# Kernel optimization log

Hardware: AMD Instinct MI355X
Metric: run time of the kernel (lower is better)

## Reference

```python
import jax, jax.numpy as jnp
import numpy as np

B, S, H0G, H1G, H0E, H1E, A, E = 16384, 512, 512, 256, 1024, 512, 64, 4


def setup_inputs() -> dict:
    key = jax.random.key(0)
    ks = jax.random.split(key, 8)
    rn = lambda k, shape, s=0.05: jax.random.normal(k, shape, jnp.float32) * s
    return {
        "x": rn(ks[0], (B, S), 1.0),
        # Gating network params (Normalizer + 2 tanh layers + fca, softmax outside)
        "g_mean": jnp.zeros((S,), jnp.float32),
        "g_std": jnp.ones((S,), jnp.float32),
        "gW0": rn(ks[1], (S, H0G)), "gb0": jnp.zeros((H0G,), jnp.float32),
        "gW1": rn(ks[2], (H0G, H1G)), "gb1": jnp.zeros((H1G,), jnp.float32),
        "gWa": rn(ks[3], (H1G, E)), "gba": jnp.zeros((E,), jnp.float32),
        # 4 expert Actors, weights stacked along leading expert axis E
        "e_mean": jnp.zeros((E, S), jnp.float32),
        "e_std": jnp.ones((E, S), jnp.float32),
        "eW0": rn(ks[4], (E, S, H0E)), "eb0": jnp.zeros((E, H0E), jnp.float32),
        "eW1": rn(ks[5], (E, H0E, H1E)), "eb1": jnp.zeros((E, H1E), jnp.float32),
        "eWa": rn(ks[6], (E, H1E, A), 0.001), "eba": jnp.zeros((E, A), jnp.float32),
        "scale": jnp.ones((A,), jnp.float32),  # (a_max - a_min) / 2
    }


def reference(x, g_mean, g_std, gW0, gb0, gW1, gb1, gWa, gba,
              e_mean, e_std, eW0, eb0, eW1, eb1, eWa, eba, scale):
    # Gating: normalize -> tanh MLP -> linear -> softmax over experts
    xg = (x - g_mean) / g_std                                   # [B,S]
    h = jnp.tanh(xg @ gW0 + gb0)
    h = jnp.tanh(h @ gW1 + gb1)
    w = jax.nn.softmax(h @ gWa + gba, axis=-1)                  # [B,E]

    # Experts (Actor.forward), batched over expert axis e
    xe = (x[None, :, :] - e_mean[:, None, :]) / e_std[:, None, :]          # [E,B,S]
    he = jnp.tanh(jnp.einsum('ebs,esh->ebh', xe, eW0) + eb0[:, None, :])   # [E,B,H0E]
    he = jnp.tanh(jnp.einsum('ebh,ehk->ebk', he, eW1) + eb1[:, None, :])   # [E,B,H1E]
    a = (jnp.einsum('ebk,eka->eba', he, eWa) + eba[:, None, :]) * scale    # [E,B,A]

    # Weighted combination of expert action means
    return jnp.einsum('be,eba->ba', w, a)                       # [B,A]
```

## Files before the change

### kernel.cpp

```cpp
#include <hip/hip_runtime.h>
#include <hip/hip_bf16.h>

typedef _Float16 f16;
typedef _Float16 f16x4 __attribute__((ext_vector_type(4)));
typedef _Float16 f16x8 __attribute__((ext_vector_type(8)));
typedef float f32x4 __attribute__((ext_vector_type(4)));

#define DEV static __device__ __forceinline__

DEV void gld_lds16(const void* g, void* l) {
  __builtin_amdgcn_global_load_lds(
      (const __attribute__((address_space(1))) void*)g,
      (__attribute__((address_space(3))) void*)l, 16, 0, 0);
}

DEV float fast_tanh(float x) {
  float e = __expf(2.0f * x);
  return 1.0f - 2.0f / (e + 1.0f);
}

DEV int xcd_swizzle(int raw, int nwg) {
  return ((nwg & 7) == 0) ? ((raw & 7) * (nwg >> 3) + (raw >> 3)) : raw;
}

__global__ __launch_bounds__(256) void k_cvt_x(const float* __restrict__ x,
                                               f16* __restrict__ xh, long n) {
  long i0 = ((long)blockIdx.x * 256 + threadIdx.x) * 4;
  long stride = (long)gridDim.x * 1024;
  for (long i = i0; i < n; i += stride) {
    const float4 v = *(const float4*)(x + i);
    f16x4 h;
    h.x = (f16)v.x; h.y = (f16)v.y; h.z = (f16)v.z; h.w = (f16)v.w;
    *(f16x4*)(xh + i) = h;
  }
}

__global__ __launch_bounds__(256) void k_transpose(const float* __restrict__ in,
                                                   f16* __restrict__ out,
                                                   const float* __restrict__ stdv,
                                                   int K_, int N_) {
  __shared__ float tile[32][33];
  const int e = blockIdx.z;
  const float* ine = in + (long)e * K_ * N_;
  f16* oute = out + (long)e * K_ * N_;
  const int n0 = blockIdx.x * 32, k0 = blockIdx.y * 32;
  const int tx = threadIdx.x, ty = threadIdx.y;
#pragma unroll
  for (int j = 0; j < 4; j++)
    tile[ty + j * 8][tx] = ine[(long)(k0 + ty + j * 8) * N_ + n0 + tx];
  __syncthreads();
  const float rs = stdv ? 1.0f / stdv[(long)e * K_ + k0 + tx] : 1.0f;
#pragma unroll
  for (int j = 0; j < 4; j++)
    oute[(long)(n0 + ty + j * 8) * K_ + k0 + tx] = (f16)(tile[tx][ty + j * 8] * rs);
}

__global__ __launch_bounds__(1024) void k_bias_corr(const float* __restrict__ W,
                                                    const float* __restrict__ b,
                                                    const float* __restrict__ mean,
                                                    const float* __restrict__ stdv,
                                                    float* __restrict__ outb,
                                                    int S_, int H_) {
  __shared__ float red[16][64];
  const int e = blockIdx.y;
  const float* We = W + (long)e * S_ * H_;
  const float* me = mean + (long)e * S_;
  const float* se = stdv + (long)e * S_;
  const int h = blockIdx.x * 64 + threadIdx.x;
  const int sl = threadIdx.y;
  float acc = 0.0f;
#pragma unroll 4
  for (int s = sl; s < S_; s += 16) acc += (me[s] / se[s]) * We[(long)s * H_ + h];
  red[sl][threadIdx.x] = acc;
  __syncthreads();
  if (sl == 0) {
    float a = 0.0f;
#pragma unroll
    for (int j = 0; j < 16; j++) a += red[j][threadIdx.x];
    outb[(long)e * H_ + h] = b[(long)e * H_ + h] - a;
  }
}

__global__ __launch_bounds__(256) void k_gemm_tanh(
    const f16* __restrict__ A, const f16* __restrict__ Bt,
    const float* __restrict__ bias, f16* __restrict__ C,
    int M, int N, int K,
    long sA, long sB, long sBias, long sC) {
  A += (long)blockIdx.z * sA; Bt += (long)blockIdx.z * sB;
  bias += (long)blockIdx.z * sBias; C += (long)blockIdx.z * sC;
  __shared__ __align__(16) f16 As[2][128 * 64];
  __shared__ __align__(16) f16 Bs[2][128 * 64];
  const int tid = threadIdx.x, wave = tid >> 6, lane = tid & 63;
  const int nwg = gridDim.x * gridDim.y;
  const int logical = xcd_swizzle(blockIdx.y * gridDim.x + blockIdx.x, nwg);
  const int bx = logical % gridDim.x, by = logical / gridDim.x;
  const int m0 = by * 128, n0 = bx * 128;
  const int wr = wave >> 1, wc = wave & 1;
  f32x4 acc[4][4] = {};
  const int swz_chunk = (tid & 7) ^ ((tid >> 3) & 7);
  const f16* Ag = A + (long)(m0 + tid / 8) * K + swz_chunk * 8;
  const f16* Bg = Bt + (long)(n0 + tid / 8) * K + swz_chunk * 8;
  const int wo = wave * 512;

#pragma unroll
  for (int i = 0; i < 4; i++) {
    gld_lds16(Ag + (long)i * 32 * K, &As[0][wo + i * 2048]);
    gld_lds16(Bg + (long)i * 32 * K, &Bs[0][wo + i * 2048]);
  }
  __syncthreads();

  const int nt = K >> 6;
  int cur = 0;
  for (int t = 0; t < nt; ++t) {
    if (t + 1 < nt) {
      const long kt = (long)(t + 1) << 6;
#pragma unroll
      for (int i = 0; i < 4; i++) {
        gld_lds16(Ag + (long)i * 32 * K + kt, &As[cur ^ 1][wo + i * 2048]);
        gld_lds16(Bg + (long)i * 32 * K + kt, &Bs[cur ^ 1][wo + i * 2048]);
      }
    }
#pragma unroll
    for (int kk = 0; kk < 2; kk++) {
      f16x8 af[4], bfr[4];
      const int rchunk = (kk * 4 + (lane >> 4)) ^ (lane & 7);
#pragma unroll
      for (int mi = 0; mi < 4; mi++)
        af[mi] = *(const f16x8*)&As[cur][(wr * 64 + mi * 16 + (lane & 15)) * 64 + rchunk * 8];
#pragma unroll
      for (int ni = 0; ni < 4; ni++)
        bfr[ni] = *(const f16x8*)&Bs[cur][(wc * 64 + ni * 16 + (lane & 15)) * 64 + rchunk * 8];
#pragma unroll
      for (int mi = 0; mi < 4; mi++)
#pragma unroll
        for (int ni = 0; ni < 4; ni++)
          acc[mi][ni] = __builtin_amdgcn_mfma_f32_16x16x32_f16(af[mi], bfr[ni], acc[mi][ni], 0, 0, 0);
    }
    __syncthreads();
    cur ^= 1;
  }

  const int r0 = (lane >> 4) * 4, cb = lane & 15;
#pragma unroll
  for (int ni = 0; ni < 4; ni++) {
    const int col = n0 + wc * 64 + ni * 16 + cb;
    const float bc = bias[col];
#pragma unroll
    for (int mi = 0; mi < 4; mi++) {
      const int row = m0 + wr * 64 + mi * 16 + r0;
#pragma unroll
      for (int r = 0; r < 4; r++)
        C[(long)(row + r) * N + col] = (f16)fast_tanh(acc[mi][ni][r] + bc);
    }
  }
}

__global__ __launch_bounds__(512, 2) void k_gemm_tanh_256(
    const f16* __restrict__ A, const f16* __restrict__ Bt,
    const float* __restrict__ bias, f16* __restrict__ C,
    const float* __restrict__ gwScale, int e0,
    int M, int N, int K,
    long sA, long sB, long sBias, long sC) {
  A += (long)blockIdx.z * sA; Bt += (long)blockIdx.z * sB;
  bias += (long)blockIdx.z * sBias; C += (long)blockIdx.z * sC;
  extern __shared__ __align__(16) f16 lds[];
  const int tid = threadIdx.x, wave = tid >> 6, lane = tid & 63;
  const int nwg = gridDim.x * gridDim.y;
  const int logical = xcd_swizzle(blockIdx.y * gridDim.x + blockIdx.x, nwg);
  const int bx = logical % gridDim.x, by = logical / gridDim.x;
  const int m0 = by * 256, n0 = bx * 256;
  const int wr = wave >> 2, wc = wave & 3;
  f32x4 acc[8][4] = {};
  const int swz_chunk = (tid & 7) ^ ((tid >> 3) & 7);
  const f16* Ag = A + (long)(m0 + tid / 8) * K + swz_chunk * 8;
  const f16* Bg = Bt + (long)(n0 + tid / 8) * K + swz_chunk * 8;
  const int wo = (wave * 8) * 64;

#pragma unroll
  for (int i = 0; i < 4; i++) {
    gld_lds16(Ag + (long)i * 64 * K, lds + wo + i * 4096);
    gld_lds16(Bg + (long)i * 64 * K, lds + 32768 + wo + i * 4096);
  }
  __syncthreads();

  const int nt = K >> 6;
  int cur = 0;
  for (int t = 0; t < nt; ++t) {
    if (t + 1 < nt) {
      const long kt = (long)(t + 1) << 6;
      f16* Ad = lds + (cur ^ 1) * 16384;
      f16* Bd = lds + 32768 + (cur ^ 1) * 16384;
#pragma unroll
      for (int i = 0; i < 4; i++) {
        gld_lds16(Ag + (long)i * 64 * K + kt, Ad + wo + i * 4096);
        gld_lds16(Bg + (long)i * 64 * K + kt, Bd + wo + i * 4096);
      }
    }
    const f16* Asc = lds + cur * 16384;
    const f16* Bsc = lds + 32768 + cur * 16384;
#pragma unroll
    for (int kk = 0; kk < 2; kk++) {
      f16x8 af[8], bfr[4];
      const int rchunk = (kk * 4 + (lane >> 4)) ^ (lane & 7);
#pragma unroll
      for (int mi = 0; mi < 8; mi++)
        af[mi] = *(const f16x8*)&Asc[(wr * 128 + mi * 16 + (lane & 15)) * 64 + rchunk * 8];
#pragma unroll
      for (int ni = 0; ni < 4; ni++)
        bfr[ni] = *(const f16x8*)&Bsc[(wc * 64 + ni * 16 + (lane & 15)) * 64 + rchunk * 8];
#pragma unroll
      for (int mi = 0; mi < 8; mi++)
#pragma unroll
        for (int ni = 0; ni < 4; ni++)
          acc[mi][ni] = __builtin_amdgcn_mfma_f32_16x16x32_f16(af[mi], bfr[ni], acc[mi][ni], 0, 0, 0);
    }
    __syncthreads();
    cur ^= 1;
  }

  const int r0 = (lane >> 4) * 4, cb = lane & 15;
  float bcv[4];
#pragma unroll
  for (int ni = 0; ni < 4; ni++) bcv[ni] = bias[n0 + wc * 64 + ni * 16 + cb];
  const int e = e0 + blockIdx.z;
#pragma unroll
  for (int mi = 0; mi < 8; mi++) {
#pragma unroll
    for (int r = 0; r < 4; r++) {
      const long row = m0 + wr * 128 + mi * 16 + r0 + r;
      const float gv = gwScale ? gwScale[row * 4 + e] : 1.0f;
#pragma unroll
      for (int ni = 0; ni < 4; ni++) {
        const int col = n0 + wc * 64 + ni * 16 + cb;
        C[row * N + col] = (f16)(fast_tanh(acc[mi][ni][r] + bcv[ni]) * gv);
      }
    }
  }
}

__global__ __launch_bounds__(256) void k_gating_head(const f16* __restrict__ h1,
                                                     const float* __restrict__ gWa,
                                                     const float* __restrict__ gba,
                                                     float* __restrict__ gw, int B_) {
  const int b = blockIdx.x * 4 + (threadIdx.x >> 6);
  const int lane = threadIdx.x & 63;
  const f16x4 hv = *(const f16x4*)&h1[(long)b * 256 + lane * 4];
  float s0 = 0, s1 = 0, s2 = 0, s3 = 0;
#pragma unroll
  for (int j = 0; j < 4; j++) {
    const float hh = (float)hv[j];
    const float4 wr4 = *(const float4*)&gWa[(lane * 4 + j) * 4];
    s0 += hh * wr4.x; s1 += hh * wr4.y; s2 += hh * wr4.z; s3 += hh * wr4.w;
  }
#pragma unroll
  for (int off = 32; off >= 1; off >>= 1) {
    s0 += __shfl_xor(s0, off);
    s1 += __shfl_xor(s1, off);
    s2 += __shfl_xor(s2, off);
    s3 += __shfl_xor(s3, off);
  }
  const float l0 = s0 + gba[0], l1 = s1 + gba[1], l2 = s2 + gba[2], l3 = s3 + gba[3];
  float mx = fmaxf(fmaxf(l0, l1), fmaxf(l2, l3));
  const float e0 = __expf(l0 - mx), e1 = __expf(l1 - mx), e2 = __expf(l2 - mx), e3 = __expf(l3 - mx);
  const float inv = 1.0f / (e0 + e1 + e2 + e3);
  if (lane == 0) {
    float4 o; o.x = e0 * inv; o.y = e1 * inv; o.z = e2 * inv; o.w = e3 * inv;
    *(float4*)&gw[(long)b * 4] = o;
  }
}

__global__ __launch_bounds__(256) void k_head_fused(const f16* __restrict__ he1,
                                                    const f16* __restrict__ Wt,
                                                    const float* __restrict__ eba,
                                                    const float* __restrict__ scale,
                                                    const float* __restrict__ gw,
                                                    float* __restrict__ out,
                                                    long sA) {
  constexpr int K = 512;
  __shared__ __align__(16) f16 As[2][64 * 64];
  __shared__ __align__(16) f16 Bs[2][64 * 64];
  const int tid = threadIdx.x, wave = tid >> 6, lane = tid & 63;
  const int bid = xcd_swizzle(blockIdx.x, gridDim.x);
  const long m0 = (long)bid * 64;
  f32x4 acc[4] = {};
  const int swz_chunk = (tid & 7) ^ ((tid >> 3) & 7);
  const f16* Ag = he1 + (m0 + tid / 8) * K + swz_chunk * 8;
  const f16* Bg = Wt + (long)(tid / 8) * K + swz_chunk * 8;
  const int wo = wave * 512;

#pragma unroll
  for (int i = 0; i < 2; i++) {
    gld_lds16(Ag + (long)i * 32 * K, &As[0][wo + i * 2048]);
    gld_lds16(Bg + (long)i * 32 * K, &Bs[0][wo + i * 2048]);
  }
  __syncthreads();
  int cur = 0;
  for (int s = 0; s < 32; ++s) {
    if (s + 1 < 32) {
      const int sn = s + 1;
      const long ae = (long)(sn >> 3) * sA + ((sn & 7) << 6);
      const long be = (long)(sn >> 3) * (64 * K) + ((sn & 7) << 6);
#pragma unroll
      for (int i = 0; i < 2; i++) {
        gld_lds16(Ag + ae + (long)i * 32 * K, &As[cur ^ 1][wo + i * 2048]);
        gld_lds16(Bg + be + (long)i * 32 * K, &Bs[cur ^ 1][wo + i * 2048]);
      }
    }
#pragma unroll
    for (int kk = 0; kk < 2; kk++) {
      const int rchunk = (kk * 4 + (lane >> 4)) ^ (lane & 7);
      const f16x8 a = *(const f16x8*)&As[cur][(wave * 16 + (lane & 15)) * 64 + rchunk * 8];
#pragma unroll
      for (int ni = 0; ni < 4; ni++) {
        const f16x8 bq = *(const f16x8*)&Bs[cur][(ni * 16 + (lane & 15)) * 64 + rchunk * 8];
        acc[ni] = __builtin_amdgcn_mfma_f32_16x16x32_f16(a, bq, acc[ni], 0, 0, 0);
      }
    }
    __syncthreads();
    cur ^= 1;
  }
  const int r0 = (lane >> 4) * 4, cb = lane & 15;
#pragma unroll
  for (int ni = 0; ni < 4; ni++) {
    const int col = ni * 16 + cb;
    const float sc = scale[col];
#pragma unroll
    for (int r = 0; r < 4; r++) {
      const long row = m0 + wave * 16 + r0 + r;
      float b4 = 0.0f;
#pragma unroll
      for (int e = 0; e < 4; e++) b4 += gw[row * 4 + e] * eba[e * 64 + col];
      out[row * 64 + col] = (acc[ni][r] + b4) * sc;
    }
  }
}

__global__ __launch_bounds__(256) void k_head(const f16* __restrict__ he1,
                                              const f16* __restrict__ Wt,
                                              const float* __restrict__ ebae,
                                              const float* __restrict__ scale,
                                              const float* __restrict__ gw,
                                              float* __restrict__ outa,
                                              int e0, int K,
                                              long sA, long sB, long sBias, long sC) {
  const int z = blockIdx.z;
  he1 += (long)z * sA; Wt += (long)z * sB; ebae += (long)z * sBias; outa += (long)z * sC;
  const int e = e0 + z;
  __shared__ __align__(16) f16 As[2][64 * 64];
  __shared__ __align__(16) f16 Bs[2][64 * 64];
  const int tid = threadIdx.x, wave = tid >> 6, lane = tid & 63;
  const int bid = xcd_swizzle(blockIdx.x, gridDim.x);
  const long m0 = (long)bid * 64;
  f32x4 acc[4] = {};
  const int swz_chunk = (tid & 7) ^ ((tid >> 3) & 7);
  const f16* Ag = he1 + (m0 + tid / 8) * K + swz_chunk * 8;
  const f16* Bg = Wt + (long)(tid / 8) * K + swz_chunk * 8;
  const int wo = wave * 512;
#pragma unroll
  for (int i = 0; i < 2; i++) {
    gld_lds16(Ag + (long)i * 32 * K, &As[0][wo + i * 2048]);
    gld_lds16(Bg + (long)i * 32 * K, &Bs[0][wo + i * 2048]);
  }
  __syncthreads();
  const int nt = K >> 6;
  int cur = 0;
  for (int t = 0; t < nt; ++t) {
    if (t + 1 < nt) {
      const long kt = (long)(t + 1) << 6;
#pragma unroll
      for (int i = 0; i < 2; i++) {
        gld_lds16(Ag + (long)i * 32 * K + kt, &As[cur ^ 1][wo + i * 2048]);
        gld_lds16(Bg + (long)i * 32 * K + kt, &Bs[cur ^ 1][wo + i * 2048]);
      }
    }
#pragma unroll
    for (int kk = 0; kk < 2; kk++) {
      const int rchunk = (kk * 4 + (lane >> 4)) ^ (lane & 7);
      const f16x8 a = *(const f16x8*)&As[cur][(wave * 16 + (lane & 15)) * 64 + rchunk * 8];
#pragma unroll
      for (int ni = 0; ni < 4; ni++) {
        const f16x8 bq = *(const f16x8*)&Bs[cur][(ni * 16 + (lane & 15)) * 64 + rchunk * 8];
        acc[ni] = __builtin_amdgcn_mfma_f32_16x16x32_f16(a, bq, acc[ni], 0, 0, 0);
      }
    }
    __syncthreads();
    cur ^= 1;
  }
  const int r0 = (lane >> 4) * 4, cb = lane & 15;
#pragma unroll
  for (int ni = 0; ni < 4; ni++) {
    const int col = ni * 16 + cb;
    const float sb = scale[col], bb = ebae[col];
    const long row0 = m0 + wave * 16 + r0;
#pragma unroll
    for (int r = 0; r < 4; r++) {
      const long row = row0 + r;
      outa[row * 64 + col] = (acc[ni][r] + bb) * sb * gw[row * 4 + e];
    }
  }
}

__global__ __launch_bounds__(256) void k_combine(const float* __restrict__ a_all,
                                                 float* __restrict__ out, long n) {
  long i = ((long)blockIdx.x * 256 + threadIdx.x) * 4;
  if (i < n) {
    const float4 v0 = *(const float4*)(a_all + i);
    const float4 v1 = *(const float4*)(a_all + n + i);
    const float4 v2 = *(const float4*)(a_all + 2 * n + i);
    const float4 v3 = *(const float4*)(a_all + 3 * n + i);
    float4 o;
    o.x = v0.x + v1.x + v2.x + v3.x;
    o.y = v0.y + v1.y + v2.y + v3.y;
    o.z = v0.z + v1.z + v2.z + v3.z;
    o.w = v0.w + v1.w + v2.w + v3.w;
    *(float4*)(out + i) = o;
  }
}

extern "C" void kernel_launch(void* const* d_in, const int* in_sizes, int n_in,
                              void* d_out, int out_size, void* d_ws, size_t ws_size,
                              hipStream_t stream) {
  constexpr int Bn = 16384, S = 512, H0G = 512, H1G = 256, H0E = 1024, H1E = 512, A = 64, E = 4;
  const float* x      = (const float*)d_in[0];
  const float* g_mean = (const float*)d_in[1];
  const float* g_std  = (const float*)d_in[2];
  const float* gW0    = (const float*)d_in[3];
  const float* gb0    = (const float*)d_in[4];
  const float* gW1    = (const float*)d_in[5];
  const float* gb1    = (const float*)d_in[6];
  const float* gWa    = (const float*)d_in[7];
  const float* gba    = (const float*)d_in[8];
  const float* e_mean = (const float*)d_in[9];
  const float* e_std  = (const float*)d_in[10];
  const float* eW0    = (const float*)d_in[11];
  const float* eb0    = (const float*)d_in[12];
  const float* eW1    = (const float*)d_in[13];
  const float* eb1    = (const float*)d_in[14];
  const float* eWa    = (const float*)d_in[15];
  const float* eba    = (const float*)d_in[16];
  const float* scale  = (const float*)d_in[17];
  float* out = (float*)d_out;

  char* p = (char*)d_ws;
  auto alloc = [&](size_t bytes) { char* q = p; p += (bytes + 255) & ~(size_t)255; return q; };
  f16* xh    = (f16*)alloc((size_t)Bn * S * 2);
  float* gw  = (float*)alloc((size_t)Bn * E * 4);
  float* a_all = (float*)alloc((size_t)E * Bn * A * 4);
  f16* gW0t  = (f16*)alloc((size_t)S * H0G * 2);
  f16* gW1t  = (f16*)alloc((size_t)H0G * H1G * 2);
  f16* eW0t  = (f16*)alloc((size_t)E * S * H0E * 2);
  f16* eW1t  = (f16*)alloc((size_t)E * H0E * H1E * 2);
  f16* eWat  = (f16*)alloc((size_t)E * H1E * A * 2);
  float* gb0c = (float*)alloc((size_t)H0G * 4);
  float* eb0c = (float*)alloc((size_t)E * H0E * 4);
  const size_t base = (size_t)(p - (char*)d_ws);
  const size_t per_g = ((size_t)Bn * H0E * 2 + 256) + ((size_t)Bn * H1E * 2 + 256);
  int g = 1;
  if (ws_size >= base + 4 * per_g) g = 4;
  else if (ws_size >= base + 2 * per_g) g = 2;
  f16* he0_g = (f16*)alloc((size_t)g * Bn * H0E * 2);
  f16* he1_g = (f16*)alloc((size_t)g * Bn * H1E * 2);
  f16* h0g = he0_g;
  f16* h1g = he1_g;

  k_cvt_x<<<2048, 256, 0, stream>>>(x, xh, (long)Bn * S);
  k_transpose<<<dim3(H0G / 32, S / 32, 1), dim3(32, 8), 0, stream>>>(gW0, gW0t, g_std, S, H0G);
  k_transpose<<<dim3(H1G / 32, H0G / 32, 1), dim3(32, 8), 0, stream>>>(gW1, gW1t, nullptr, H0G, H1G);
  k_transpose<<<dim3(H0E / 32, S / 32, E), dim3(32, 8), 0, stream>>>(eW0, eW0t, e_std, S, H0E);
  k_transpose<<<dim3(H1E / 32, H0E / 32, E), dim3(32, 8), 0, stream>>>(eW1, eW1t, nullptr, H0E, H1E);
  k_transpose<<<dim3(A / 32, H1E / 32, E), dim3(32, 8), 0, stream>>>(eWa, eWat, nullptr, H1E, A);
  k_bias_corr<<<dim3(H0G / 64, 1), dim3(64, 16), 0, stream>>>(gW0, gb0, g_mean, g_std, gb0c, S, H0G);
  k_bias_corr<<<dim3(H0E / 64, E), dim3(64, 16), 0, stream>>>(eW0, eb0, e_mean, e_std, eb0c, S, H0E);

  k_gemm_tanh<<<dim3(H0G / 128, Bn / 128), 256, 0, stream>>>(
      xh, gW0t, gb0c, h0g, Bn, H0G, S, 0, 0, 0, 0);
  k_gemm_tanh<<<dim3(H1G / 128, Bn / 128), 256, 0, stream>>>(
      h0g, gW1t, gb1, h1g, Bn, H1G, H0G, 0, 0, 0, 0);
  k_gating_head<<<Bn / 4, 256, 0, stream>>>(h1g, gWa, gba, gw, Bn);

  constexpr size_t LDS256 = 2 * 2 * 256 * 64 * sizeof(f16);
  if (g == 4) {
    k_gemm_tanh_256<<<dim3(H0E / 256, Bn / 256, 4), 512, LDS256, stream>>>(
        xh, eW0t, eb0c, he0_g, nullptr, 0,
        Bn, H0E, S, 0, (long)S * H0E, H0E, (long)Bn * H0E);
    k_gemm_tanh_256<<<dim3(H1E / 256, Bn / 256, 4), 512, LDS256, stream>>>(
        he0_g, eW1t, eb1, he1_g, gw, 0,
        Bn, H1E, H0E, (long)Bn * H0E, (long)H0E * H1E, H1E, (long)Bn * H1E);
    k_head_fused<<<dim3(Bn / 64), 256, 0, stream>>>(
        he1_g, eWat, eba, scale, gw, out, (long)Bn * H1E);
  } else {
    for (int e0 = 0; e0 < E; e0 += g) {
      k_gemm_tanh_256<<<dim3(H0E / 256, Bn / 256, g), 512, LDS256, stream>>>(
          xh, eW0t + (size_t)e0 * S * H0E, eb0c + (size_t)e0 * H0E, he0_g, nullptr, 0,
          Bn, H0E, S, 0, (long)S * H0E, H0E, (long)Bn * H0E);
      k_gemm_tanh_256<<<dim3(H1E / 256, Bn / 256, g), 512, LDS256, stream>>>(
          he0_g, eW1t + (size_t)e0 * H0E * H1E, eb1 + (size_t)e0 * H1E, he1_g, nullptr, 0,
          Bn, H1E, H0E, (long)Bn * H0E, (long)H0E * H1E, H1E, (long)Bn * H1E);
      k_head<<<dim3(Bn / 64, 1, g), 256, 0, stream>>>(
          he1_g, eWat + (size_t)e0 * H1E * A, eba + (size_t)e0 * A, scale, gw,
          a_all + (size_t)e0 * Bn * A, e0, H1E,
          (long)Bn * H1E, (long)H1E * A, A, (long)Bn * A);
    }
    k_combine<<<(Bn * A) / 1024, 256, 0, stream>>>(a_all, out, (long)Bn * A);
  }
}
```

Baseline: 302.6 us.

## Replace double-buffered expert GEMM with 4-stage K=32 LDS ring pipeline

The 256x256 expert GEMM kernel moves from a double-buffered K=64 tile loop to a four-slot ring of K=32 tiles, with three tiles in flight. Partial vmcnt waits plus a raw s_barrier replace the full __syncthreads, so global-to-LDS loads overlap MFMA work more deeply. MFMA issue is split into halves under raised s_setprio, and the LDS chunk swizzle is changed for the narrower tile. The cost is more barriers per K (one per 32 instead of per 64) and hand-counted waitcnt logic that is fragile.

Result: no change. 306.2 us (+1.2%).

```diff
diff --git a/kernel.cpp b/kernel.cpp
--- a/kernel.cpp
+++ b/kernel.cpp
@@ -155,7 +155,7 @@
   }
 }
 
-__global__ __launch_bounds__(512, 2) void k_gemm_tanh_256(
+__global__ __launch_bounds__(512, 2) void k_gemm_ring(
     const f16* __restrict__ A, const f16* __restrict__ Bt,
     const float* __restrict__ bias, f16* __restrict__ C,
     const float* __restrict__ gwScale, int e0,
@@ -171,52 +171,81 @@
   const int m0 = by * 256, n0 = bx * 256;
   const int wr = wave >> 2, wc = wave & 3;
   f32x4 acc[8][4] = {};
-  const int swz_chunk = (tid & 7) ^ ((tid >> 3) & 7);
-  const f16* Ag = A + (long)(m0 + tid / 8) * K + swz_chunk * 8;
-  const f16* Bg = Bt + (long)(n0 + tid / 8) * K + swz_chunk * 8;
-  const int wo = (wave * 8) * 64;
-
-#pragma unroll
-  for (int i = 0; i < 4; i++) {
-    gld_lds16(Ag + (long)i * 64 * K, lds + wo + i * 4096);
-    gld_lds16(Bg + (long)i * 64 * K, lds + 32768 + wo + i * 4096);
-  }
-  __syncthreads();
-
-  const int nt = K >> 6;
-  int cur = 0;
+
+  const int c = ((lane & 3) - ((lane >> 3) & 3)) & 3;
+  const int srow = wave * 32 + (lane >> 2);
+  const f16* Ag = A + (long)(m0 + srow) * K + c * 8;
+  const f16* Bg = Bt + (long)(n0 + srow) * K + c * 8;
+  const int wdst = wave * 1024;
+
+  const int pc = ((lane >> 4) + ((lane >> 1) & 3)) & 3;
+  const int arow = wr * 128 + (lane & 15);
+  const int brow = wc * 64 + (lane & 15);
+
+#define STAGE(tile)                                                   \
+  {                                                                   \
+    f16* _la = lds + ((tile) & 3) * 16384;                            \
+    f16* _lb = _la + 8192;                                            \
+    const long _kt = (long)(tile) << 5;                               \
+    gld_lds16(Ag + _kt, _la + wdst);                                  \
+    gld_lds16(Ag + _kt + (long)16 * K, _la + wdst + 512);             \
+    gld_lds16(Bg + _kt, _lb + wdst);                                  \
+    gld_lds16(Bg + _kt + (long)16 * K, _lb + wdst + 512);             \
+  }
+
+  const int nt = K >> 5;
+  STAGE(0); STAGE(1); STAGE(2);
+  asm volatile("s_waitcnt vmcnt(8)" ::: "memory");
+  __builtin_amdgcn_s_barrier();
+  asm volatile("" ::: "memory");
+
   for (int t = 0; t < nt; ++t) {
-    if (t + 1 < nt) {
-      const long kt = (long)(t + 1) << 6;
-      f16* Ad = lds + (cur ^ 1) * 16384;
-      f16* Bd = lds + 32768 + (cur ^ 1) * 16384;
-#pragma unroll
-      for (int i = 0; i < 4; i++) {
-        gld_lds16(Ag + (long)i * 64 * K + kt, Ad + wo + i * 4096);
-        gld_lds16(Bg + (long)i * 64 * K + kt, Bd + wo + i * 4096);
-      }
-    }
-    const f16* Asc = lds + cur * 16384;
-    const f16* Bsc = lds + 32768 + cur * 16384;
-#pragma unroll
-    for (int kk = 0; kk < 2; kk++) {
-      f16x8 af[8], bfr[4];
-      const int rchunk = (kk * 4 + (lane >> 4)) ^ (lane & 7);
-#pragma unroll
-      for (int mi = 0; mi < 8; mi++)
-        af[mi] = *(const f16x8*)&Asc[(wr * 128 + mi * 16 + (lane & 15)) * 64 + rchunk * 8];
-#pragma unroll
-      for (int ni = 0; ni < 4; ni++)
-        bfr[ni] = *(const f16x8*)&Bsc[(wc * 64 + ni * 16 + (lane & 15)) * 64 + rchunk * 8];
-#pragma unroll
-      for (int mi = 0; mi < 8; mi++)
-#pragma unroll
-        for (int ni = 0; ni < 4; ni++)
-          acc[mi][ni] = __builtin_amdgcn_mfma_f32_16x16x32_f16(af[mi], bfr[ni], acc[mi][ni], 0, 0, 0);
-    }
-    __syncthreads();
-    cur ^= 1;
-  }
+    if (t + 3 < nt) STAGE(t + 3);
+    const f16* Abuf = lds + (t & 3) * 16384;
+    const f16* Bbuf = Abuf + 8192;
+    f16x8 af[8], bfr[4];
+#pragma unroll
+    for (int mi = 0; mi < 4; mi++)
+      af[mi] = *(const f16x8*)&Abuf[(arow + mi * 16) * 32 + pc * 8];
+#pragma unroll
+    for (int ni = 0; ni < 2; ni++)
+      bfr[ni] = *(const f16x8*)&Bbuf[(brow + ni * 16) * 32 + pc * 8];
+    __builtin_amdgcn_s_setprio(1);
+#pragma unroll
+    for (int mi = 0; mi < 4; mi++)
+#pragma unroll
+      for (int ni = 0; ni < 2; ni++)
+        acc[mi][ni] = __builtin_amdgcn_mfma_f32_16x16x32_f16(af[mi], bfr[ni], acc[mi][ni], 0, 0, 0);
+    __builtin_amdgcn_s_setprio(0);
+#pragma unroll
+    for (int mi = 4; mi < 8; mi++)
+      af[mi] = *(const f16x8*)&Abuf[(arow + mi * 16) * 32 + pc * 8];
+#pragma unroll
+    for (int ni = 2; ni < 4; ni++)
+      bfr[ni] = *(const f16x8*)&Bbuf[(brow + ni * 16) * 32 + pc * 8];
+    __builtin_amdgcn_s_setprio(1);
+#pragma unroll
+    for (int mi = 4; mi < 8; mi++)
+#pragma unroll
+      for (int ni = 0; ni < 2; ni++)
+        acc[mi][ni] = __builtin_amdgcn_mfma_f32_16x16x32_f16(af[mi], bfr[ni], acc[mi][ni], 0, 0, 0);
+#pragma unroll
+    for (int mi = 0; mi < 8; mi++)
+#pragma unroll
+      for (int ni = 2; ni < 4; ni++)
+        acc[mi][ni] = __builtin_amdgcn_mfma_f32_16x16x32_f16(af[mi], bfr[ni], acc[mi][ni], 0, 0, 0);
+    __builtin_amdgcn_s_setprio(0);
+    if (t + 3 < nt) {
+      asm volatile("s_waitcnt vmcnt(8)" ::: "memory");
+    } else if (t + 2 < nt) {
+      asm volatile("s_waitcnt vmcnt(4)" ::: "memory");
+    } else {
+      asm volatile("s_waitcnt vmcnt(0)" ::: "memory");
+    }
+    __builtin_amdgcn_s_barrier();
+    asm volatile("" ::: "memory");
+  }
+#undef STAGE
 
   const int r0 = (lane >> 4) * 4, cb = lane & 15;
   float bcv[4];
@@ -376,7 +405,7 @@
 #pragma unroll
     for (int kk = 0; kk < 2; kk++) {
       const int rchunk = (kk * 4 + (lane >> 4)) ^ (lane & 7);
-      const f16x8 a = *(const f16x8*)&As[cur][(wave * 16 + (lane & 15)) * 64 + rchunk * 8];
+      const f16x8 a = *(const f16x8*)&As[cur][(wave * 16 + (lane & 15)) * 64 + kk * 0 + rchunk * 8];
 #pragma unroll
       for (int ni = 0; ni < 4; ni++) {
         const f16x8 bq = *(const f16x8*)&Bs[cur][(ni * 16 + (lane & 15)) * 64 + rchunk * 8];
@@ -478,22 +507,22 @@
       h0g, gW1t, gb1, h1g, Bn, H1G, H0G, 0, 0, 0, 0);
   k_gating_head<<<Bn / 4, 256, 0, stream>>>(h1g, gWa, gba, gw, Bn);
 
-  constexpr size_t LDS256 = 2 * 2 * 256 * 64 * sizeof(f16);
+  constexpr size_t LDSRING = 4 * 2 * 256 * 32 * sizeof(f16);
   if (g == 4) {
-    k_gemm_tanh_256<<<dim3(H0E / 256, Bn / 256, 4), 512, LDS256, stream>>>(
+    k_gemm_ring<<<dim3(H0E / 256, Bn / 256, 4), 512, LDSRING, stream>>>(
         xh, eW0t, eb0c, he0_g, nullptr, 0,
         Bn, H0E, S, 0, (long)S * H0E, H0E, (long)Bn * H0E);
-    k_gemm_tanh_256<<<dim3(H1E / 256, Bn / 256, 4), 512, LDS256, stream>>>(
+    k_gemm_ring<<<dim3(H1E / 256, Bn / 256, 4), 512, LDSRING, stream>>>(
         he0_g, eW1t, eb1, he1_g, gw, 0,
         Bn, H1E, H0E, (long)Bn * H0E, (long)H0E * H1E, H1E, (long)Bn * H1E);
     k_head_fused<<<dim3(Bn / 64), 256, 0, stream>>>(
         he1_g, eWat, eba, scale, gw, out, (long)Bn * H1E);
   } else {
     for (int e0 = 0; e0 < E; e0 += g) {
-      k_gemm_tanh_256<<<dim3(H0E / 256, Bn / 256, g), 512, LDS256, stream>>>(
+      k_gemm_ring<<<dim3(H0E / 256, Bn / 256, g), 512, LDSRING, stream>>>(
           xh, eW0t + (size_t)e0 * S * H0E, eb0c + (size_t)e0 * H0E, he0_g, nullptr, 0,
           Bn, H0E, S, 0, (long)S * H0E, H0E, (long)Bn * H0E);
-      k_gemm_tanh_256<<<dim3(H1E / 256, Bn / 256, g), 512, LDS256, stream>>>(
+      k_gemm_ring<<<dim3(H1E / 256, Bn / 256, g), 512, LDSRING, stream>>>(
           he0_g, eW1t + (size_t)e0 * H0E * H1E, eb1 + (size_t)e0 * H1E, he1_g, nullptr, 0,
           Bn, H1E, H0E, (long)Bn * H0E, (long)H0E * H1E, H1E, (long)Bn * H1E);
       k_head<<<dim3(Bn / 64, 1, g), 256, 0, stream>>>(
```

## Rewrite expert GEMM with 8-phase interleaved LDS pipeline and concatenated layer-0 weights

Applied to the files above, without the earlier changes.

Replaces the double-buffered expert GEMM main loop with an explicitly scheduled 8-phase loop. Global-to-LDS staging is split into halves and interleaved with MFMA sub-blocks, with explicit barriers, waitcnts and s_setprio raised around MFMA bursts. The layer-0 expert GEMM now runs as one wide GEMM over all experts' concatenated weights (N = E*H0E), writing an interleaved [B, E*H0E] activation that layer 1 reads with a leading dimension. The aim is better overlap of memory traffic with matrix math and better reuse of the shared input tile. The added barriers could serialize waves, and the unrolled schedule assumes K is a multiple of 128.

New measurement: 444.3 us. 46.8% more time.

```diff
diff --git a/kernel.cpp b/kernel.cpp
--- a/kernel.cpp
+++ b/kernel.cpp
@@ -155,11 +155,11 @@
   }
 }
 
-__global__ __launch_bounds__(512, 2) void k_gemm_tanh_256(
+__global__ __launch_bounds__(512, 2) void k_gemm_8ph(
     const f16* __restrict__ A, const f16* __restrict__ Bt,
     const float* __restrict__ bias, f16* __restrict__ C,
     const float* __restrict__ gwScale, int e0,
-    int M, int N, int K,
+    int M, int K, int lda, int ldb, int ldc,
     long sA, long sB, long sBias, long sC) {
   A += (long)blockIdx.z * sA; Bt += (long)blockIdx.z * sB;
   bias += (long)blockIdx.z * sBias; C += (long)blockIdx.z * sC;
@@ -171,52 +171,96 @@
   const int m0 = by * 256, n0 = bx * 256;
   const int wr = wave >> 2, wc = wave & 3;
   f32x4 acc[8][4] = {};
-  const int swz_chunk = (tid & 7) ^ ((tid >> 3) & 7);
-  const f16* Ag = A + (long)(m0 + tid / 8) * K + swz_chunk * 8;
-  const f16* Bg = Bt + (long)(n0 + tid / 8) * K + swz_chunk * 8;
-  const int wo = (wave * 8) * 64;
-
-#pragma unroll
-  for (int i = 0; i < 4; i++) {
-    gld_lds16(Ag + (long)i * 64 * K, lds + wo + i * 4096);
-    gld_lds16(Bg + (long)i * 64 * K, lds + 32768 + wo + i * 4096);
-  }
-  __syncthreads();
-
-  const int nt = K >> 6;
-  int cur = 0;
-  for (int t = 0; t < nt; ++t) {
-    if (t + 1 < nt) {
-      const long kt = (long)(t + 1) << 6;
-      f16* Ad = lds + (cur ^ 1) * 16384;
-      f16* Bd = lds + 32768 + (cur ^ 1) * 16384;
-#pragma unroll
-      for (int i = 0; i < 4; i++) {
-        gld_lds16(Ag + (long)i * 64 * K + kt, Ad + wo + i * 4096);
-        gld_lds16(Bg + (long)i * 64 * K + kt, Bd + wo + i * 4096);
-      }
-    }
-    const f16* Asc = lds + cur * 16384;
-    const f16* Bsc = lds + 32768 + cur * 16384;
-#pragma unroll
-    for (int kk = 0; kk < 2; kk++) {
-      f16x8 af[8], bfr[4];
-      const int rchunk = (kk * 4 + (lane >> 4)) ^ (lane & 7);
-#pragma unroll
-      for (int mi = 0; mi < 8; mi++)
-        af[mi] = *(const f16x8*)&Asc[(wr * 128 + mi * 16 + (lane & 15)) * 64 + rchunk * 8];
-#pragma unroll
-      for (int ni = 0; ni < 4; ni++)
-        bfr[ni] = *(const f16x8*)&Bsc[(wc * 64 + ni * 16 + (lane & 15)) * 64 + rchunk * 8];
-#pragma unroll
-      for (int mi = 0; mi < 8; mi++)
-#pragma unroll
-        for (int ni = 0; ni < 4; ni++)
-          acc[mi][ni] = __builtin_amdgcn_mfma_f32_16x16x32_f16(af[mi], bfr[ni], acc[mi][ni], 0, 0, 0);
-    }
-    __syncthreads();
-    cur ^= 1;
-  }
+
+  const int swz = (tid & 7) ^ ((tid >> 3) & 7);
+  const f16* Ag = A + (long)(m0 + (tid >> 3)) * lda + swz * 8;
+  const f16* Bg = Bt + (long)(n0 + (tid >> 3)) * ldb + swz * 8;
+  const int wst = wave * 512;
+
+  const int rA0 = (lane >> 4) ^ (lane & 7);
+  const int rA1 = (4 + (lane >> 4)) ^ (lane & 7);
+  int aoff[8], boff[4];
+#pragma unroll
+  for (int mi = 0; mi < 8; mi++) aoff[mi] = (wr * 128 + mi * 16 + (lane & 15)) * 64;
+#pragma unroll
+  for (int ni = 0; ni < 4; ni++) boff[ni] = 16384 + (wc * 64 + ni * 16 + (lane & 15)) * 64;
+
+#define STG_A(buf, rh, tile)                                                      \
+  gld_lds16(Ag + (long)((rh)*128) * lda + (long)(tile) * 64,                      \
+            lds + (buf) * 32768 + (rh) * 8192 + wst);                             \
+  gld_lds16(Ag + (long)((rh)*128 + 64) * lda + (long)(tile) * 64,                 \
+            lds + (buf) * 32768 + (rh) * 8192 + 4096 + wst);
+#define STG_B(buf, rh, tile)                                                      \
+  gld_lds16(Bg + (long)((rh)*128) * ldb + (long)(tile) * 64,                      \
+            lds + (buf) * 32768 + 16384 + (rh) * 8192 + wst);                     \
+  gld_lds16(Bg + (long)((rh)*128 + 64) * ldb + (long)(tile) * 64,                 \
+            lds + (buf) * 32768 + 16384 + (rh) * 8192 + 4096 + wst);
+#define LOAD_A(buf, rc)                                                           \
+  _Pragma("unroll") for (int mi = 0; mi < 8; mi++)                                \
+      af[mi] = *(const f16x8*)&lds[(buf) * 32768 + aoff[mi] + (rc) * 8];
+#define LOAD_B2(buf, nb, rc)                                                      \
+  bfr[0] = *(const f16x8*)&lds[(buf) * 32768 + boff[(nb)*2] + (rc) * 8];          \
+  bfr[1] = *(const f16x8*)&lds[(buf) * 32768 + boff[(nb)*2 + 1] + (rc) * 8];
+#define MMA(nb)                                                                   \
+  __builtin_amdgcn_s_setprio(1);                                                  \
+  _Pragma("unroll") for (int mi = 0; mi < 8; mi++) {                              \
+    acc[mi][(nb)*2] =                                                             \
+        __builtin_amdgcn_mfma_f32_16x16x32_f16(af[mi], bfr[0], acc[mi][(nb)*2], 0, 0, 0); \
+    acc[mi][(nb)*2 + 1] =                                                         \
+        __builtin_amdgcn_mfma_f32_16x16x32_f16(af[mi], bfr[1], acc[mi][(nb)*2 + 1], 0, 0, 0); \
+  }                                                                               \
+  __builtin_amdgcn_s_setprio(0);
+#define BAR()                          \
+  __builtin_amdgcn_s_barrier();        \
+  asm volatile("" ::: "memory")
+#define WAITL()                                          \
+  asm volatile("s_waitcnt lgkmcnt(0)" ::: "memory");     \
+  __builtin_amdgcn_sched_barrier(0)
+#define WAITV() asm volatile("s_waitcnt vmcnt(0)" ::: "memory")
+
+  const int nkt = K >> 6;
+  const int niter = nkt >> 1;
+
+  STG_A(0, 0, 0) STG_A(0, 1, 0) STG_B(0, 0, 0) STG_B(0, 1, 0)
+  WAITV();
+  BAR();
+
+  f16x8 af[8], bfr[2];
+  for (int t = 0; t < niter; ++t) {
+    const int kt1 = 2 * t + 1;
+    LOAD_A(0, rA0) LOAD_B2(0, 0, rA0)
+    STG_A(1, 0, kt1) STG_A(1, 1, kt1)
+    BAR(); WAITL(); MMA(0) BAR();
+    LOAD_B2(0, 1, rA0)
+    STG_B(1, 0, kt1) STG_B(1, 1, kt1)
+    BAR(); WAITL(); MMA(1) BAR();
+    LOAD_A(0, rA1) LOAD_B2(0, 0, rA1)
+    BAR(); WAITL(); MMA(0) BAR();
+    LOAD_B2(0, 1, rA1)
+    BAR(); WAITL(); MMA(1)
+    WAITV();
+    BAR();
+    LOAD_A(1, rA0) LOAD_B2(1, 0, rA0)
+    if (kt1 + 1 < nkt) { STG_A(0, 0, kt1 + 1) STG_A(0, 1, kt1 + 1) }
+    BAR(); WAITL(); MMA(0) BAR();
+    LOAD_B2(1, 1, rA0)
+    if (kt1 + 1 < nkt) { STG_B(0, 0, kt1 + 1) STG_B(0, 1, kt1 + 1) }
+    BAR(); WAITL(); MMA(1) BAR();
+    LOAD_A(1, rA1) LOAD_B2(1, 0, rA1)
+    BAR(); WAITL(); MMA(0) BAR();
+    LOAD_B2(1, 1, rA1)
+    BAR(); WAITL(); MMA(1)
+    WAITV();
+    BAR();
+  }
+#undef STG_A
+#undef STG_B
+#undef LOAD_A
+#undef LOAD_B2
+#undef MMA
+#undef BAR
+#undef WAITL
+#undef WAITV
 
   const int r0 = (lane >> 4) * 4, cb = lane & 15;
   float bcv[4];
@@ -232,7 +276,7 @@
 #pragma unroll
       for (int ni = 0; ni < 4; ni++) {
         const int col = n0 + wc * 64 + ni * 16 + cb;
-        C[row * N + col] = (f16)(fast_tanh(acc[mi][ni][r] + bcv[ni]) * gv);
+        C[row * (long)ldc + col] = (f16)(fast_tanh(acc[mi][ni][r] + bcv[ni]) * gv);
       }
     }
   }
@@ -478,24 +522,26 @@
       h0g, gW1t, gb1, h1g, Bn, H1G, H0G, 0, 0, 0, 0);
   k_gating_head<<<Bn / 4, 256, 0, stream>>>(h1g, gWa, gba, gw, Bn);
 
-  constexpr size_t LDS256 = 2 * 2 * 256 * 64 * sizeof(f16);
+  constexpr size_t LDS8 = 2 * 2 * 256 * 64 * sizeof(f16);
   if (g == 4) {
-    k_gemm_tanh_256<<<dim3(H0E / 256, Bn / 256, 4), 512, LDS256, stream>>>(
+    k_gemm_8ph<<<dim3((E * H0E) / 256, Bn / 256, 1), 512, LDS8, stream>>>(
         xh, eW0t, eb0c, he0_g, nullptr, 0,
-        Bn, H0E, S, 0, (long)S * H0E, H0E, (long)Bn * H0E);
-    k_gemm_tanh_256<<<dim3(H1E / 256, Bn / 256, 4), 512, LDS256, stream>>>(
+        Bn, S, S, S, E * H0E, 0, 0, 0, 0);
+    k_gemm_8ph<<<dim3(H1E / 256, Bn / 256, E), 512, LDS8, stream>>>(
         he0_g, eW1t, eb1, he1_g, gw, 0,
-        Bn, H1E, H0E, (long)Bn * H0E, (long)H0E * H1E, H1E, (long)Bn * H1E);
+        Bn, H0E, E * H0E, H0E, H1E,
+        H0E, (long)H0E * H1E, H1E, (long)Bn * H1E);
     k_head_fused<<<dim3(Bn / 64), 256, 0, stream>>>(
         he1_g, eWat, eba, scale, gw, out, (long)Bn * H1E);
   } else {
     for (int e0 = 0; e0 < E; e0 += g) {
-      k_gemm_tanh_256<<<dim3(H0E / 256, Bn / 256, g), 512, LDS256, stream>>>(
+      k_gemm_8ph<<<dim3(H0E / 256, Bn / 256, g), 512, LDS8, stream>>>(
           xh, eW0t + (size_t)e0 * S * H0E, eb0c + (size_t)e0 * H0E, he0_g, nullptr, 0,
-          Bn, H0E, S, 0, (long)S * H0E, H0E, (long)Bn * H0E);
-      k_gemm_tanh_256<<<dim3(H1E / 256, Bn / 256, g), 512, LDS256, stream>>>(
+          Bn, S, S, S, H0E, 0, (long)S * H0E, H0E, (long)Bn * H0E);
+      k_gemm_8ph<<<dim3(H1E / 256, Bn / 256, g), 512, LDS8, stream>>>(
           he0_g, eW1t + (size_t)e0 * H0E * H1E, eb1 + (size_t)e0 * H1E, he1_g, nullptr, 0,
-          Bn, H1E, H0E, (long)Bn * H0E, (long)H0E * H1E, H1E, (long)Bn * H1E);
+          Bn, H0E, H0E, H0E, H1E,
+          (long)Bn * H0E, (long)H0E * H1E, H1E, (long)Bn * H1E);
       k_head<<<dim3(Bn / 64, 1, g), 256, 0, stream>>>(
           he1_g, eWat + (size_t)e0 * H1E * A, eba + (size_t)e0 * A, scale, gw,
           a_all + (size_t)e0 * Bn * A, e0, H1E,
```

## Replace 256x256 K64 expert GEMM with 128x128 K32 tile kernel

Applied to the files above, without the earlier changes.

Swaps the 512-thread 256x256 expert GEMM (64-wide K steps, dynamic LDS) for a 256-thread 128x128 kernel that uses 32-wide K steps, static double-buffered LDS, a new XOR swizzle and occupancy 4. The goal is more resident workgroups and better latency hiding and wave balance across CUs. In exchange, operand reuse per tile drops, so more global and LDS traffic is needed per FLOP, and the shorter K step means more barriers per unit of work. It also adds explicit lda/ldb/ldc stride parameters.

Result: slower. 332.4 us (+9.8%).

```diff
diff --git a/kernel.cpp b/kernel.cpp
--- a/kernel.cpp
+++ b/kernel.cpp
@@ -155,84 +155,71 @@
   }
 }
 
-__global__ __launch_bounds__(512, 2) void k_gemm_tanh_256(
+__global__ __launch_bounds__(256, 4) void k_gemm32(
     const f16* __restrict__ A, const f16* __restrict__ Bt,
     const float* __restrict__ bias, f16* __restrict__ C,
     const float* __restrict__ gwScale, int e0,
-    int M, int N, int K,
+    int M, int K, int lda, int ldb, int ldc,
     long sA, long sB, long sBias, long sC) {
   A += (long)blockIdx.z * sA; Bt += (long)blockIdx.z * sB;
   bias += (long)blockIdx.z * sBias; C += (long)blockIdx.z * sC;
-  extern __shared__ __align__(16) f16 lds[];
+  __shared__ __align__(16) f16 As[2][128 * 32];
+  __shared__ __align__(16) f16 Bs[2][128 * 32];
   const int tid = threadIdx.x, wave = tid >> 6, lane = tid & 63;
   const int nwg = gridDim.x * gridDim.y;
   const int logical = xcd_swizzle(blockIdx.y * gridDim.x + blockIdx.x, nwg);
   const int bx = logical % gridDim.x, by = logical / gridDim.x;
-  const int m0 = by * 256, n0 = bx * 256;
-  const int wr = wave >> 2, wc = wave & 3;
-  f32x4 acc[8][4] = {};
-  const int swz_chunk = (tid & 7) ^ ((tid >> 3) & 7);
-  const f16* Ag = A + (long)(m0 + tid / 8) * K + swz_chunk * 8;
-  const f16* Bg = Bt + (long)(n0 + tid / 8) * K + swz_chunk * 8;
-  const int wo = (wave * 8) * 64;
-
-#pragma unroll
-  for (int i = 0; i < 4; i++) {
-    gld_lds16(Ag + (long)i * 64 * K, lds + wo + i * 4096);
-    gld_lds16(Bg + (long)i * 64 * K, lds + 32768 + wo + i * 4096);
-  }
-  __syncthreads();
-
-  const int nt = K >> 6;
+  const int m0 = by * 128, n0 = bx * 128;
+  const int wr = wave >> 1, wc = wave & 1;
+  f32x4 acc[4][4] = {};
+  const int sc = (tid & 3) ^ ((tid >> 2) & 3) ^ ((tid >> 4) & 3);
+  const f16* Ag = A + (long)(m0 + (tid >> 2)) * lda + sc * 8;
+  const f16* Bg = Bt + (long)(n0 + (tid >> 2)) * ldb + sc * 8;
+  const int wst = wave * 512;
+  const int rc = ((lane >> 4) ^ (lane & 3) ^ ((lane >> 2) & 3)) * 8;
+
+#define STG(buf, t)                                                          \
+  gld_lds16(Ag + (long)(t) * 32, &As[buf][wst]);                             \
+  gld_lds16(Ag + (long)64 * lda + (long)(t) * 32, &As[buf][wst + 2048]);     \
+  gld_lds16(Bg + (long)(t) * 32, &Bs[buf][wst]);                             \
+  gld_lds16(Bg + (long)64 * ldb + (long)(t) * 32, &Bs[buf][wst + 2048]);
+
+  const int nt = K >> 5;
+  STG(0, 0)
+  __syncthreads();
   int cur = 0;
   for (int t = 0; t < nt; ++t) {
-    if (t + 1 < nt) {
-      const long kt = (long)(t + 1) << 6;
-      f16* Ad = lds + (cur ^ 1) * 16384;
-      f16* Bd = lds + 32768 + (cur ^ 1) * 16384;
-#pragma unroll
-      for (int i = 0; i < 4; i++) {
-        gld_lds16(Ag + (long)i * 64 * K + kt, Ad + wo + i * 4096);
-        gld_lds16(Bg + (long)i * 64 * K + kt, Bd + wo + i * 4096);
-      }
-    }
-    const f16* Asc = lds + cur * 16384;
-    const f16* Bsc = lds + 32768 + cur * 16384;
-#pragma unroll
-    for (int kk = 0; kk < 2; kk++) {
-      f16x8 af[8], bfr[4];
-      const int rchunk = (kk * 4 + (lane >> 4)) ^ (lane & 7);
-#pragma unroll
-      for (int mi = 0; mi < 8; mi++)
-        af[mi] = *(const f16x8*)&Asc[(wr * 128 + mi * 16 + (lane & 15)) * 64 + rchunk * 8];
+    if (t + 1 < nt) { STG(cur ^ 1, t + 1) }
+    f16x8 af[4], bfr[4];
+#pragma unroll
+    for (int mi = 0; mi < 4; mi++)
+      af[mi] = *(const f16x8*)&As[cur][(wr * 64 + mi * 16 + (lane & 15)) * 32 + rc];
+#pragma unroll
+    for (int ni = 0; ni < 4; ni++)
+      bfr[ni] = *(const f16x8*)&Bs[cur][(wc * 64 + ni * 16 + (lane & 15)) * 32 + rc];
+#pragma unroll
+    for (int mi = 0; mi < 4; mi++)
 #pragma unroll
       for (int ni = 0; ni < 4; ni++)
-        bfr[ni] = *(const f16x8*)&Bsc[(wc * 64 + ni * 16 + (lane & 15)) * 64 + rchunk * 8];
-#pragma unroll
-      for (int mi = 0; mi < 8; mi++)
-#pragma unroll
-        for (int ni = 0; ni < 4; ni++)
-          acc[mi][ni] = __builtin_amdgcn_mfma_f32_16x16x32_f16(af[mi], bfr[ni], acc[mi][ni], 0, 0, 0);
-    }
+        acc[mi][ni] = __builtin_amdgcn_mfma_f32_16x16x32_f16(af[mi], bfr[ni], acc[mi][ni], 0, 0, 0);
     __syncthreads();
     cur ^= 1;
   }
+#undef STG
 
   const int r0 = (lane >> 4) * 4, cb = lane & 15;
-  float bcv[4];
-#pragma unroll
-  for (int ni = 0; ni < 4; ni++) bcv[ni] = bias[n0 + wc * 64 + ni * 16 + cb];
   const int e = e0 + blockIdx.z;
 #pragma unroll
-  for (int mi = 0; mi < 8; mi++) {
-#pragma unroll
-    for (int r = 0; r < 4; r++) {
-      const long row = m0 + wr * 128 + mi * 16 + r0 + r;
-      const float gv = gwScale ? gwScale[row * 4 + e] : 1.0f;
-#pragma unroll
-      for (int ni = 0; ni < 4; ni++) {
-        const int col = n0 + wc * 64 + ni * 16 + cb;
-        C[row * N + col] = (f16)(fast_tanh(acc[mi][ni][r] + bcv[ni]) * gv);
+  for (int ni = 0; ni < 4; ni++) {
+    const int col = n0 + wc * 64 + ni * 16 + cb;
+    const float bc = bias[col];
+#pragma unroll
+    for (int mi = 0; mi < 4; mi++) {
+      const int row = m0 + wr * 64 + mi * 16 + r0;
+#pragma unroll
+      for (int r = 0; r < 4; r++) {
+        const float gv = gwScale ? gwScale[(long)(row + r) * 4 + e] : 1.0f;
+        C[(long)(row + r) * ldc + col] = (f16)(fast_tanh(acc[mi][ni][r] + bc) * gv);
       }
     }
   }
@@ -478,24 +465,27 @@
       h0g, gW1t, gb1, h1g, Bn, H1G, H0G, 0, 0, 0, 0);
   k_gating_head<<<Bn / 4, 256, 0, stream>>>(h1g, gWa, gba, gw, Bn);
 
-  constexpr size_t LDS256 = 2 * 2 * 256 * 64 * sizeof(f16);
   if (g == 4) {
-    k_gemm_tanh_256<<<dim3(H0E / 256, Bn / 256, 4), 512, LDS256, stream>>>(
+    k_gemm32<<<dim3(H0E / 128, Bn / 128, 4), 256, 0, stream>>>(
         xh, eW0t, eb0c, he0_g, nullptr, 0,
-        Bn, H0E, S, 0, (long)S * H0E, H0E, (long)Bn * H0E);
-    k_gemm_tanh_256<<<dim3(H1E / 256, Bn / 256, 4), 512, LDS256, stream>>>(
+        Bn, S, S, S, H0E,
+        0, (long)S * H0E, H0E, (long)Bn * H0E);
+    k_gemm32<<<dim3(H1E / 128, Bn / 128, 4), 256, 0, stream>>>(
         he0_g, eW1t, eb1, he1_g, gw, 0,
-        Bn, H1E, H0E, (long)Bn * H0E, (long)H0E * H1E, H1E, (long)Bn * H1E);
+        Bn, H0E, H0E, H0E, H1E,
+        (long)Bn * H0E, (long)H0E * H1E, H1E, (long)Bn * H1E);
     k_head_fused<<<dim3(Bn / 64), 256, 0, stream>>>(
         he1_g, eWat, eba, scale, gw, out, (long)Bn * H1E);
   } else {
     for (int e0 = 0; e0 < E; e0 += g) {
-      k_gemm_tanh_256<<<dim3(H0E / 256, Bn / 256, g), 512, LDS256, stream>>>(
+      k_gemm32<<<dim3(H0E / 128, Bn / 128, g), 256, 0, stream>>>(
           xh, eW0t + (size_t)e0 * S * H0E, eb0c + (size_t)e0 * H0E, he0_g, nullptr, 0,
-          Bn, H0E, S, 0, (long)S * H0E, H0E, (long)Bn * H0E);
-      k_gemm_tanh_256<<<dim3(H1E / 256, Bn / 256, g), 512, LDS256, stream>>>(
+          Bn, S, S, S, H0E,
+          0, (long)S * H0E, H0E, (long)Bn * H0E);
+      k_gemm32<<<dim3(H1E / 128, Bn / 128, g), 256, 0, stream>>>(
           he0_g, eW1t + (size_t)e0 * H0E * H1E, eb1 + (size_t)e0 * H1E, he1_g, nullptr, 0,
-          Bn, H1E, H0E, (long)Bn * H0E, (long)H0E * H1E, H1E, (long)Bn * H1E);
+          Bn, H0E, H0E, H0E, H1E,
+          (long)Bn * H0E, (long)H0E * H1E, H1E, (long)Bn * H1E);
       k_head<<<dim3(Bn / 64, 1, g), 256, 0, stream>>>(
           he1_g, eWat + (size_t)e0 * H1E * A, eba + (size_t)e0 * A, scale, gw,
           a_all + (size_t)e0 * Bn * A, e0, H1E,
```
